# Performance work log

Hardware: AMD Instinct MI355X
Metric: run time of the kernel (lower is better)

The kernel has to match this reference:

```python
import jax, jax.numpy as jnp
import numpy as np

B, S, D = 1, 4096, 512
INNER = 512
K, PAD = 3, 1
MAX_OUT = 4 * S  # static padded output length (torch uses data-dependent max)
EPS = 1e-5
TINY_SLOWDOWN = 0.5


def _conv1d(x, w, b):
    # x: [B, C_in, S], w: [C_out, C_in, K] -> [B, C_out, S]
    y = jax.lax.conv_general_dilated(x, w, window_strides=(1,), padding=[(PAD, PAD)],
                                     dimension_numbers=('NCH', 'OIH', 'NCH'))
    return y + b[None, :, None]


def _layernorm(x, g, b):
    m = jnp.mean(x, axis=-1, keepdims=True)
    v = jnp.var(x, axis=-1, keepdims=True)
    return (x - m) * jax.lax.rsqrt(v + EPS) * g + b


def _duration_predictor(enc, c1w, c1b, g1, b1, c2w, c2b, g2, b2, lw, lb):
    # enc: [B, S, D]; dropout is identity (eval mode)
    x = _conv1d(enc.transpose(0, 2, 1), c1w, c1b).transpose(0, 2, 1)   # [B,S,INNER]
    x = jax.nn.relu(_layernorm(x, g1, b1))
    x = _conv1d(x.transpose(0, 2, 1), c2w, c2b).transpose(0, 2, 1)     # [B,S,INNER]
    x = jax.nn.relu(_layernorm(x, g2, b2))
    out = jax.nn.relu(jnp.einsum('bsd,od->bso', x, lw) + lb)           # [B,S,1]
    return out[..., 0]                                                  # [B,S] (B==1 => matches squeeze/unsqueeze(0))


def setup_inputs() -> dict:
    key = jax.random.key(0)
    ks = jax.random.split(key, 4)
    return {
        'enc_output': jax.random.normal(ks[0], (B, S, D), dtype=jnp.float32),
        'conv1_w': jax.random.normal(ks[1], (INNER, D, K), dtype=jnp.float32) * 0.02,
        'conv1_b': jnp.zeros((INNER,), jnp.float32),
        'ln1_g': jnp.ones((INNER,), jnp.float32),
        'ln1_b': jnp.zeros((INNER,), jnp.float32),
        'conv2_w': jax.random.normal(ks[2], (INNER, INNER, K), dtype=jnp.float32) * 0.02,
        'conv2_b': jnp.zeros((INNER,), jnp.float32),
        'ln2_g': jnp.ones((INNER,), jnp.float32),
        'ln2_b': jnp.zeros((INNER,), jnp.float32),
        'lin_w': jax.random.normal(ks[3], (1, INNER), jnp.float32) * 0.1,
        'lin_b': jnp.zeros((1,), jnp.float32),
    }


def reference(enc_output, conv1_w, conv1_b, ln1_g, ln1_b, conv2_w, conv2_b,
              ln2_g, ln2_b, lin_w, lin_b):
    pred = _duration_predictor(enc_output, conv1_w, conv1_b, ln1_g, ln1_b,
                               conv2_w, conv2_b, ln2_g, ln2_b, lin_w, lin_b)
    dur = jnp.floor(pred + TINY_SLOWDOWN).astype(jnp.int32)            # [B,S], nonneg so floor == int()
    cum = jnp.cumsum(dur, axis=-1)                                     # [B,S]
    t = jnp.arange(MAX_OUT, dtype=jnp.int32)                           # [T]
    # frame t belongs to phoneme i where cum[i-1] <= t < cum[i]
    idx = jax.vmap(lambda c: jnp.searchsorted(c, t, side='right'))(cum)  # [B,T]
    valid = t[None, :] < cum[:, -1:]                                   # [B,T]
    idx = jnp.clip(idx, 0, S - 1)
    gathered = jnp.take_along_axis(enc_output, idx[:, :, None], axis=1)  # [B,T,D]
    mod_enc_output = jnp.where(valid[:, :, None], gathered, jnp.zeros((), enc_output.dtype))
    output_pos = jnp.arange(1, MAX_OUT + 1, dtype=jnp.int64 if jax.config.jax_enable_x64 else jnp.int32)[None, :]
    return mod_enc_output, output_pos
```

## Files before the change

kernel.cpp:

```cpp
#include <hip/hip_runtime.h>

#define S      4096
#define D      512
#define KWIN   3
#define SP     (S + 2)
#define MAXOUT 16384
#define EPSLN  1e-5f
#define NIT    16
#define NKT    48
#define KSPLIT 2
#define KHALF  (NKT / KSPLIT)

typedef __attribute__((ext_vector_type(8)))  short short8;
typedef __attribute__((ext_vector_type(16))) float floatx16;

__device__ inline ushort f2bf(float x) {
  union { float f; unsigned u; } v; v.f = x;
  unsigned r = v.u + 0x7fffu + ((v.u >> 16) & 1u);
  return (ushort)(r >> 16);
}
__device__ inline float bf2f(ushort h) {
  union { float f; unsigned u; } v; v.u = ((unsigned)h) << 16;
  return v.f;
}

#define NB0 1025
#define NB1 384
#define NB3 4

__device__ inline void wpack8(const float* __restrict__ w, ushort* __restrict__ bh,
                              ushort* __restrict__ bl, int q) {
  const int kk0 = (q & 3) * 8;
  const int o   = (q >> 2) & 511;
  const int it  = (q >> 11) & 15;
  const int k   = q >> 15;
  short8 h8, l8;
#pragma unroll
  for (int j = 0; j < 8; ++j) {
    const float v = w[o * (D * KWIN) + (it * 32 + kk0 + j) * KWIN + k];
    const ushort hi = f2bf(v);
    h8[j] = (short)hi;
    l8[j] = (short)f2bf(v - bf2f(hi));
  }
  *(short8*)(bh + (size_t)q * 8) = h8;
  *(short8*)(bl + (size_t)q * 8) = l8;
}

__global__ __launch_bounds__(256) void pack_all_kernel(
    const float* __restrict__ x, const float* __restrict__ w1,
    const float* __restrict__ w2, ushort* __restrict__ Xph,
    ushort* __restrict__ Xpl, ushort* __restrict__ B1h, ushort* __restrict__ B1l,
    ushort* __restrict__ B2h, ushort* __restrict__ B2l,
    ushort* __restrict__ T1h, ushort* __restrict__ T1l) {
  const int b = blockIdx.x;
  if (b < NB0) {
    const int t = b * 256 + threadIdx.x;
    if (t >= SP * 64) return;
    const int g  = t >> 6;
    const int i0 = (t & 63) * 8;
    float vv[8] = {};
    if (g > 0 && g < SP - 1) {
      const float4 v0 = *(const float4*)(x + (size_t)(g - 1) * D + i0);
      const float4 v1 = *(const float4*)(x + (size_t)(g - 1) * D + i0 + 4);
      vv[0] = v0.x; vv[1] = v0.y; vv[2] = v0.z; vv[3] = v0.w;
      vv[4] = v1.x; vv[5] = v1.y; vv[6] = v1.z; vv[7] = v1.w;
    }
    short8 h8, l8;
#pragma unroll
    for (int j = 0; j < 8; ++j) {
      const ushort hi = f2bf(vv[j]);
      h8[j] = (short)hi;
      l8[j] = (short)f2bf(vv[j] - bf2f(hi));
    }
    const size_t dst = ((size_t)(i0 >> 5) * SP + g) * 32 + (i0 & 31);
    *(short8*)(Xph + dst) = h8;
    *(short8*)(Xpl + dst) = l8;
  } else if (b < NB0 + NB1) {
    wpack8(w1, B1h, B1l, (b - NB0) * 256 + threadIdx.x);
  } else if (b < NB0 + 2 * NB1) {
    wpack8(w2, B2h, B2l, (b - NB0 - NB1) * 256 + threadIdx.x);
  } else {
    const int idx = (b - NB0 - 2 * NB1) * 256 + threadIdx.x;
    const int c   = idx >> 6;
    const int rr  = (idx >> 5) & 1;
    const int col = idx & 31;
    const size_t off = ((size_t)c * SP + (rr ? (SP - 1) : 0)) * 32 + col;
    T1h[off] = 0;
    T1l[off] = 0;
  }
}

__device__ inline void gload16(const void* g, void* l) {
  __builtin_amdgcn_global_load_lds((const __attribute__((address_space(1))) void*)g,
                                   (__attribute__((address_space(3))) void*)l,
                                   16, 0, 0);
}

__global__ __launch_bounds__(256) void gemm_mfma_kernel(
    const ushort* __restrict__ Ah, const ushort* __restrict__ Al,
    const ushort* __restrict__ Bh, const ushort* __restrict__ Bl,
    float* __restrict__ C0, float* __restrict__ C1) {
  __shared__ __align__(16) ushort smem[2][4][128 * 32];

  const int tid  = threadIdx.x;
  const int wave = tid >> 6;
  const int lane = tid & 63;
  const int row0 = blockIdx.x * 128;
  const int col0 = blockIdx.y * 128;
  const int ktb  = blockIdx.z * KHALF;
  const int wm0  = (wave >> 1) * 64;
  const int wn0  = (wave & 1) * 64;
  const int ln31 = lane & 31;
  const int half = lane >> 5;

  floatx16 acc[2][2] = {};

  auto stage = [&](int stg, int db) {
    const int kt    = ktb + stg;
    const int tap   = kt >> 4;
    const int itile = kt & 15;
    const ushort* gb;
    if (wave == 0)      gb = Ah + ((size_t)itile * SP + row0 + tap) * 32;
    else if (wave == 1) gb = Al + ((size_t)itile * SP + row0 + tap) * 32;
    else if (wave == 2) gb = Bh + ((size_t)kt * D + col0) * 32;
    else                gb = Bl + ((size_t)kt * D + col0) * 32;
    ushort* lb = &smem[db][wave][0];
#pragma unroll
    for (int seg = 0; seg < 8; ++seg) {
      const int r = seg * 16 + (lane >> 2);
      const int c = (lane & 3) ^ (r & 3);
      gload16(gb + (size_t)r * 32 + c * 8, lb + seg * 512);
    }
  };

  stage(0, 0);

  for (int p = 0; p < KHALF; ++p) {
    const int db = p & 1;
    __syncthreads();
    if (p + 1 < KHALF) stage(p + 1, db ^ 1);

#pragma unroll
    for (int sub = 0; sub < 2; ++sub) {
      const int cchunk = sub * 2 + half;
      short8 ah[2], al2[2], bh[2], bl2[2];
#pragma unroll
      for (int mf = 0; mf < 2; ++mf) {
        const int r  = wm0 + mf * 32 + ln31;
        const int cs = cchunk ^ (r & 3);
        const int off = r * 32 + cs * 8;
        ah[mf]  = *(const short8*)&smem[db][0][off];
        al2[mf] = *(const short8*)&smem[db][1][off];
      }
#pragma unroll
      for (int nf = 0; nf < 2; ++nf) {
        const int r  = wn0 + nf * 32 + ln31;
        const int cs = cchunk ^ (r & 3);
        const int off = r * 32 + cs * 8;
        bh[nf]  = *(const short8*)&smem[db][2][off];
        bl2[nf] = *(const short8*)&smem[db][3][off];
      }
#pragma unroll
      for (int mf = 0; mf < 2; ++mf)
#pragma unroll
        for (int nf = 0; nf < 2; ++nf) {
          acc[mf][nf] = __builtin_amdgcn_mfma_f32_32x32x16_bf16(ah[mf],  bh[nf],  acc[mf][nf], 0, 0, 0);
          acc[mf][nf] = __builtin_amdgcn_mfma_f32_32x32x16_bf16(ah[mf],  bl2[nf], acc[mf][nf], 0, 0, 0);
          acc[mf][nf] = __builtin_amdgcn_mfma_f32_32x32x16_bf16(al2[mf], bh[nf],  acc[mf][nf], 0, 0, 0);
        }
    }
  }

  float* C = (blockIdx.z == 0) ? C0 : C1;
#pragma unroll
  for (int mf = 0; mf < 2; ++mf)
#pragma unroll
    for (int nf = 0; nf < 2; ++nf) {
      const int col = col0 + wn0 + nf * 32 + ln31;
#pragma unroll
      for (int reg = 0; reg < 16; ++reg) {
        const int row = row0 + wm0 + mf * 32 + (reg & 3) + 8 * (reg >> 2) + 4 * half;
        C[(size_t)row * D + col] = acc[mf][nf][reg];
      }
    }
}

__global__ __launch_bounds__(256) void ln_relu_pack_kernel(
    const float* __restrict__ X0, const float* __restrict__ X1,
    const float* __restrict__ cb, const float* __restrict__ gam,
    const float* __restrict__ bet, ushort* __restrict__ th,
    ushort* __restrict__ tl) {
  const int wave = threadIdx.x >> 6;
  const int lane = threadIdx.x & 63;
  const int s = blockIdx.x * 4 + wave;
  const float4* x0p = (const float4*)(X0 + (size_t)s * D);
  const float4* x1p = (const float4*)(X1 + (size_t)s * D);
  const float4 a0 = x0p[2 * lane],     b0 = x0p[2 * lane + 1];
  const float4 a1 = x1p[2 * lane],     b1 = x1p[2 * lane + 1];
  const float4 ca  = ((const float4*)cb)[2 * lane];
  const float4 cb2 = ((const float4*)cb)[2 * lane + 1];
  float v[8] = {(a0.x + a1.x) + ca.x,  (a0.y + a1.y) + ca.y,
                (a0.z + a1.z) + ca.z,  (a0.w + a1.w) + ca.w,
                (b0.x + b1.x) + cb2.x, (b0.y + b1.y) + cb2.y,
                (b0.z + b1.z) + cb2.z, (b0.w + b1.w) + cb2.w};
  float sum = 0.f;
#pragma unroll
  for (int i = 0; i < 8; ++i) sum += v[i];
#pragma unroll
  for (int off = 32; off > 0; off >>= 1) sum += __shfl_xor(sum, off);
  const float m = sum * (1.0f / D);
  float sq = 0.f;
#pragma unroll
  for (int i = 0; i < 8; ++i) { v[i] -= m; sq += v[i] * v[i]; }
#pragma unroll
  for (int off = 32; off > 0; off >>= 1) sq += __shfl_xor(sq, off);
  const float rs = rsqrtf(sq * (1.0f / D) + EPSLN);
  const float4 ga = ((const float4*)gam)[2 * lane];
  const float4 gb = ((const float4*)gam)[2 * lane + 1];
  const float4 ba = ((const float4*)bet)[2 * lane];
  const float4 bb = ((const float4*)bet)[2 * lane + 1];
  const float gg[8] = {ga.x, ga.y, ga.z, ga.w, gb.x, gb.y, gb.z, gb.w};
  const float bt[8] = {ba.x, ba.y, ba.z, ba.w, bb.x, bb.y, bb.z, bb.w};
  short8 h8, l8;
#pragma unroll
  for (int i = 0; i < 8; ++i) {
    const float y = fmaxf(v[i] * rs * gg[i] + bt[i], 0.0f);
    const ushort hi = f2bf(y);
    h8[i] = (short)hi;
    l8[i] = (short)f2bf(y - bf2f(hi));
  }
  const size_t base = ((size_t)(lane >> 2) * SP + (s + 1)) * 32 + (size_t)(lane & 3) * 8;
  *(short8*)(th + base) = h8;
  *(short8*)(tl + base) = l8;
}

__global__ __launch_bounds__(256) void ln2_pred_kernel(
    const float* __restrict__ X0, const float* __restrict__ X1,
    const float* __restrict__ cb, const float* __restrict__ gam,
    const float* __restrict__ bet, const float* __restrict__ lw,
    const float* __restrict__ lb, int* __restrict__ dur) {
  const int wave = threadIdx.x >> 6;
  const int lane = threadIdx.x & 63;
  const int s = blockIdx.x * 4 + wave;
  const float4* x0p = (const float4*)(X0 + (size_t)s * D);
  const float4* x1p = (const float4*)(X1 + (size_t)s * D);
  const float4 a0 = x0p[2 * lane],     b0 = x0p[2 * lane + 1];
  const float4 a1 = x1p[2 * lane],     b1 = x1p[2 * lane + 1];
  const float4 ca  = ((const float4*)cb)[2 * lane];
  const float4 cb2 = ((const float4*)cb)[2 * lane + 1];
  float v[8] = {(a0.x + a1.x) + ca.x,  (a0.y + a1.y) + ca.y,
                (a0.z + a1.z) + ca.z,  (a0.w + a1.w) + ca.w,
                (b0.x + b1.x) + cb2.x, (b0.y + b1.y) + cb2.y,
                (b0.z + b1.z) + cb2.z, (b0.w + b1.w) + cb2.w};
  float sum = 0.f;
#pragma unroll
  for (int i = 0; i < 8; ++i) sum += v[i];
#pragma unroll
  for (int off = 32; off > 0; off >>= 1) sum += __shfl_xor(sum, off);
  const float m = sum * (1.0f / D);
  float sq = 0.f;
#pragma unroll
  for (int i = 0; i < 8; ++i) { v[i] -= m; sq += v[i] * v[i]; }
#pragma unroll
  for (int off = 32; off > 0; off >>= 1) sq += __shfl_xor(sq, off);
  const float rs = rsqrtf(sq * (1.0f / D) + EPSLN);
  const float4 ga = ((const float4*)gam)[2 * lane];
  const float4 gb = ((const float4*)gam)[2 * lane + 1];
  const float4 ba = ((const float4*)bet)[2 * lane];
  const float4 bb = ((const float4*)bet)[2 * lane + 1];
  const float gg[8] = {ga.x, ga.y, ga.z, ga.w, gb.x, gb.y, gb.z, gb.w};
  const float bt[8] = {ba.x, ba.y, ba.z, ba.w, bb.x, bb.y, bb.z, bb.w};
  const float4 w0 = ((const float4*)lw)[2 * lane];
  const float4 w1 = ((const float4*)lw)[2 * lane + 1];
  const float ww[8] = {w0.x, w0.y, w0.z, w0.w, w1.x, w1.y, w1.z, w1.w};
  float d = 0.f;
#pragma unroll
  for (int i = 0; i < 8; ++i) {
    const float y = fmaxf(v[i] * rs * gg[i] + bt[i], 0.0f);
    d += y * ww[i];
  }
#pragma unroll
  for (int off = 32; off > 0; off >>= 1) d += __shfl_xor(d, off);
  if (lane == 0) {
    const float p = fmaxf(d + lb[0], 0.0f);
    dur[s] = (int)floorf(p + 0.5f);
  }
}

__global__ __launch_bounds__(64) void scan_kernel(const int* __restrict__ dur,
                                                  int* __restrict__ cum) {
  const int lane = threadIdx.x;
  const int4* src = (const int4*)dur + (size_t)lane * 16;
  int4 v[16];
  int run = 0;
#pragma unroll
  for (int i = 0; i < 16; ++i) {
    int4 d = src[i];
    d.x += run; d.y += d.x; d.z += d.y; d.w += d.z;
    run = d.w;
    v[i] = d;
  }
  int sc = run;
#pragma unroll
  for (int off = 1; off < 64; off <<= 1) {
    const int n = __shfl_up(sc, off);
    if (lane >= off) sc += n;
  }
  const int base = sc - run;
  int4* dst = (int4*)cum + (size_t)lane * 16;
#pragma unroll
  for (int i = 0; i < 16; ++i) {
    int4 d = v[i];
    d.x += base; d.y += base; d.z += base; d.w += base;
    dst[i] = d;
  }
}

__global__ __launch_bounds__(256) void gather_kernel(
    const float* __restrict__ enc, const int* __restrict__ cum,
    float* __restrict__ out0, float* __restrict__ out1) {
  const int half = threadIdx.x >> 7;
  const int d4   = (threadIdx.x & 127) << 2;
  const int t    = blockIdx.x * 2 + half;
  const int total = cum[S - 1];

  int lo = 0, hi = S;
  while (lo < hi) {
    const int mid = (lo + hi) >> 1;
    if (cum[mid] <= t) lo = mid + 1; else hi = mid;
  }
  const int idx = (lo < S) ? lo : (S - 1);

  float4 v = make_float4(0.f, 0.f, 0.f, 0.f);
  if (t < total) v = *(const float4*)(enc + (size_t)idx * D + d4);
  *(float4*)(out0 + (size_t)t * D + d4) = v;

  if ((threadIdx.x & 127) == 0) out1[t] = (float)(t + 1);
}

extern "C" void kernel_launch(void* const* d_in, const int* in_sizes, int n_in,
                              void* d_out, int out_size, void* d_ws, size_t ws_size,
                              hipStream_t stream) {
  const float* enc = (const float*)d_in[0];
  const float* w1  = (const float*)d_in[1];
  const float* cb1 = (const float*)d_in[2];
  const float* g1  = (const float*)d_in[3];
  const float* be1 = (const float*)d_in[4];
  const float* w2  = (const float*)d_in[5];
  const float* cb2 = (const float*)d_in[6];
  const float* g2  = (const float*)d_in[7];
  const float* be2 = (const float*)d_in[8];
  const float* lw  = (const float*)d_in[9];
  const float* lb  = (const float*)d_in[10];

  float* out0 = (float*)d_out;
  float* out1 = out0 + (size_t)MAXOUT * D;

  const size_t NP = (size_t)NIT * SP * 32;
  const size_t NB = (size_t)NKT * D * 32;
  ushort* Xph = (ushort*)d_ws;
  ushort* Xpl = Xph + NP;
  ushort* T1h = Xpl + NP;
  ushort* T1l = T1h + NP;
  ushort* B1h = T1l + NP;
  ushort* B1l = B1h + NB;
  ushort* B2h = B1l + NB;
  ushort* B2l = B2h + NB;
  float*  t0a = (float*)(B2l + NB);
  float*  t0b = t0a + (size_t)S * D;
  int*   dur  = (int*)(t0b + (size_t)S * D);
  int*   cum  = dur + S;

  pack_all_kernel<<<NB0 + 2 * NB1 + NB3, 256, 0, stream>>>(
      enc, w1, w2, Xph, Xpl, B1h, B1l, B2h, B2l, T1h, T1l);
  gemm_mfma_kernel<<<dim3(S / 128, D / 128, KSPLIT), 256, 0, stream>>>(
      Xph, Xpl, B1h, B1l, t0a, t0b);
  ln_relu_pack_kernel<<<S / 4, 256, 0, stream>>>(t0a, t0b, cb1, g1, be1, T1h, T1l);
  gemm_mfma_kernel<<<dim3(S / 128, D / 128, KSPLIT), 256, 0, stream>>>(
      T1h, T1l, B2h, B2l, t0a, t0b);
  ln2_pred_kernel<<<S / 4, 256, 0, stream>>>(t0a, t0b, cb2, g2, be2, lw, lb, dur);
  scan_kernel<<<1, 64, 0, stream>>>(dur, cum);
  gather_kernel<<<MAXOUT / 2, 256, 0, stream>>>(enc, cum, out0, out1);
}
```

Measured before the change: 170.6 us.

## Split GEMM K dimension four ways and switch LDS tile to column-chunk layout

Raises the split-K factor from 2 to 4, so each GEMM launches 512 blocks instead of 256 and can fill more compute units. The LN kernels now sum four partial outputs. The LDS staging layout changes from a per-row XOR-swizzled layout to a chunk-major layout, so each lane reads 16 contiguous bytes per row. The cost is twice as much fp32 partial-result traffic to and from global memory, plus a different LDS bank-access pattern.

```diff
diff --git a/kernel.cpp b/kernel.cpp
--- a/kernel.cpp
+++ b/kernel.cpp
@@ -8,8 +8,8 @@
 #define EPSLN  1e-5f
 #define NIT    16
 #define NKT    48
-#define KSPLIT 2
-#define KHALF  (NKT / KSPLIT)
+#define KSPLIT 4
+#define KQ     (NKT / KSPLIT)
 
 typedef __attribute__((ext_vector_type(8)))  short short8;
 typedef __attribute__((ext_vector_type(16))) float floatx16;
@@ -99,15 +99,15 @@
 __global__ __launch_bounds__(256) void gemm_mfma_kernel(
     const ushort* __restrict__ Ah, const ushort* __restrict__ Al,
     const ushort* __restrict__ Bh, const ushort* __restrict__ Bl,
-    float* __restrict__ C0, float* __restrict__ C1) {
-  __shared__ __align__(16) ushort smem[2][4][128 * 32];
+    float* __restrict__ Cpart) {
+  __shared__ __align__(16) ushort smem[2][4][4096];
 
   const int tid  = threadIdx.x;
   const int wave = tid >> 6;
   const int lane = tid & 63;
   const int row0 = blockIdx.x * 128;
   const int col0 = blockIdx.y * 128;
-  const int ktb  = blockIdx.z * KHALF;
+  const int ktb  = blockIdx.z * KQ;
   const int wm0  = (wave >> 1) * 64;
   const int wn0  = (wave & 1) * 64;
   const int ln31 = lane & 31;
@@ -127,38 +127,38 @@
     ushort* lb = &smem[db][wave][0];
 #pragma unroll
     for (int seg = 0; seg < 8; ++seg) {
-      const int r = seg * 16 + (lane >> 2);
-      const int c = (lane & 3) ^ (r & 3);
+      const int r = (seg & 1) * 64 + lane;
+      const int c = seg >> 1;
       gload16(gb + (size_t)r * 32 + c * 8, lb + seg * 512);
     }
   };
 
   stage(0, 0);
 
-  for (int p = 0; p < KHALF; ++p) {
+  for (int p = 0; p < KQ; ++p) {
     const int db = p & 1;
     __syncthreads();
-    if (p + 1 < KHALF) stage(p + 1, db ^ 1);
-
+    if (p + 1 < KQ) stage(p + 1, db ^ 1);
+
+    const ushort* Ahs = &smem[db][0][0];
+    const ushort* Als = &smem[db][1][0];
+    const ushort* Bhs = &smem[db][2][0];
+    const ushort* Bls = &smem[db][3][0];
 #pragma unroll
     for (int sub = 0; sub < 2; ++sub) {
-      const int cchunk = sub * 2 + half;
+      const int cc = sub * 2 + half;
       short8 ah[2], al2[2], bh[2], bl2[2];
 #pragma unroll
       for (int mf = 0; mf < 2; ++mf) {
-        const int r  = wm0 + mf * 32 + ln31;
-        const int cs = cchunk ^ (r & 3);
-        const int off = r * 32 + cs * 8;
-        ah[mf]  = *(const short8*)&smem[db][0][off];
-        al2[mf] = *(const short8*)&smem[db][1][off];
+        const int off = (cc * 128 + wm0 + mf * 32 + ln31) * 8;
+        ah[mf]  = *(const short8*)&Ahs[off];
+        al2[mf] = *(const short8*)&Als[off];
       }
 #pragma unroll
       for (int nf = 0; nf < 2; ++nf) {
-        const int r  = wn0 + nf * 32 + ln31;
-        const int cs = cchunk ^ (r & 3);
-        const int off = r * 32 + cs * 8;
-        bh[nf]  = *(const short8*)&smem[db][2][off];
-        bl2[nf] = *(const short8*)&smem[db][3][off];
+        const int off = (cc * 128 + wn0 + nf * 32 + ln31) * 8;
+        bh[nf]  = *(const short8*)&Bhs[off];
+        bl2[nf] = *(const short8*)&Bls[off];
       }
 #pragma unroll
       for (int mf = 0; mf < 2; ++mf)
@@ -171,7 +171,7 @@
     }
   }
 
-  float* C = (blockIdx.z == 0) ? C0 : C1;
+  float* C = Cpart + (size_t)blockIdx.z * S * D;
 #pragma unroll
   for (int mf = 0; mf < 2; ++mf)
 #pragma unroll
@@ -185,24 +185,28 @@
     }
 }
 
+__device__ inline void load8(const float* p, int lane, float o[8]) {
+  const float4 a = ((const float4*)p)[2 * lane];
+  const float4 b = ((const float4*)p)[2 * lane + 1];
+  o[0] = a.x; o[1] = a.y; o[2] = a.z; o[3] = a.w;
+  o[4] = b.x; o[5] = b.y; o[6] = b.z; o[7] = b.w;
+}
+
 __global__ __launch_bounds__(256) void ln_relu_pack_kernel(
-    const float* __restrict__ X0, const float* __restrict__ X1,
-    const float* __restrict__ cb, const float* __restrict__ gam,
-    const float* __restrict__ bet, ushort* __restrict__ th,
-    ushort* __restrict__ tl) {
+    const float* __restrict__ Xp, const float* __restrict__ cb,
+    const float* __restrict__ gam, const float* __restrict__ bet,
+    ushort* __restrict__ th, ushort* __restrict__ tl) {
   const int wave = threadIdx.x >> 6;
   const int lane = threadIdx.x & 63;
   const int s = blockIdx.x * 4 + wave;
-  const float4* x0p = (const float4*)(X0 + (size_t)s * D);
-  const float4* x1p = (const float4*)(X1 + (size_t)s * D);
-  const float4 a0 = x0p[2 * lane],     b0 = x0p[2 * lane + 1];
-  const float4 a1 = x1p[2 * lane],     b1 = x1p[2 * lane + 1];
-  const float4 ca  = ((const float4*)cb)[2 * lane];
-  const float4 cb2 = ((const float4*)cb)[2 * lane + 1];
-  float v[8] = {(a0.x + a1.x) + ca.x,  (a0.y + a1.y) + ca.y,
-                (a0.z + a1.z) + ca.z,  (a0.w + a1.w) + ca.w,
-                (b0.x + b1.x) + cb2.x, (b0.y + b1.y) + cb2.y,
-                (b0.z + b1.z) + cb2.z, (b0.w + b1.w) + cb2.w};
+  float v[8], x1[8], x2[8], x3[8], bi[8];
+  load8(Xp + (size_t)s * D, lane, v);
+  load8(Xp + (size_t)S * D + (size_t)s * D, lane, x1);
+  load8(Xp + 2 * (size_t)S * D + (size_t)s * D, lane, x2);
+  load8(Xp + 3 * (size_t)S * D + (size_t)s * D, lane, x3);
+  load8(cb, lane, bi);
+#pragma unroll
+  for (int i = 0; i < 8; ++i) v[i] = ((v[i] + x1[i]) + (x2[i] + x3[i])) + bi[i];
   float sum = 0.f;
 #pragma unroll
   for (int i = 0; i < 8; ++i) sum += v[i];
@@ -215,12 +219,9 @@
 #pragma unroll
   for (int off = 32; off > 0; off >>= 1) sq += __shfl_xor(sq, off);
   const float rs = rsqrtf(sq * (1.0f / D) + EPSLN);
-  const float4 ga = ((const float4*)gam)[2 * lane];
-  const float4 gb = ((const float4*)gam)[2 * lane + 1];
-  const float4 ba = ((const float4*)bet)[2 * lane];
-  const float4 bb = ((const float4*)bet)[2 * lane + 1];
-  const float gg[8] = {ga.x, ga.y, ga.z, ga.w, gb.x, gb.y, gb.z, gb.w};
-  const float bt[8] = {ba.x, ba.y, ba.z, ba.w, bb.x, bb.y, bb.z, bb.w};
+  float gg[8], bt[8];
+  load8(gam, lane, gg);
+  load8(bet, lane, bt);
   short8 h8, l8;
 #pragma unroll
   for (int i = 0; i < 8; ++i) {
@@ -235,23 +236,21 @@
 }
 
 __global__ __launch_bounds__(256) void ln2_pred_kernel(
-    const float* __restrict__ X0, const float* __restrict__ X1,
-    const float* __restrict__ cb, const float* __restrict__ gam,
-    const float* __restrict__ bet, const float* __restrict__ lw,
-    const float* __restrict__ lb, int* __restrict__ dur) {
+    const float* __restrict__ Xp, const float* __restrict__ cb,
+    const float* __restrict__ gam, const float* __restrict__ bet,
+    const float* __restrict__ lw, const float* __restrict__ lb,
+    int* __restrict__ dur) {
   const int wave = threadIdx.x >> 6;
   const int lane = threadIdx.x & 63;
   const int s = blockIdx.x * 4 + wave;
-  const float4* x0p = (const float4*)(X0 + (size_t)s * D);
-  const float4* x1p = (const float4*)(X1 + (size_t)s * D);
-  const float4 a0 = x0p[2 * lane],     b0 = x0p[2 * lane + 1];
-  const float4 a1 = x1p[2 * lane],     b1 = x1p[2 * lane + 1];
-  const float4 ca  = ((const float4*)cb)[2 * lane];
-  const float4 cb2 = ((const float4*)cb)[2 * lane + 1];
-  float v[8] = {(a0.x + a1.x) + ca.x,  (a0.y + a1.y) + ca.y,
-                (a0.z + a1.z) + ca.z,  (a0.w + a1.w) + ca.w,
-                (b0.x + b1.x) + cb2.x, (b0.y + b1.y) + cb2.y,
-                (b0.z + b1.z) + cb2.z, (b0.w + b1.w) + cb2.w};
+  float v[8], x1[8], x2[8], x3[8], bi[8];
+  load8(Xp + (size_t)s * D, lane, v);
+  load8(Xp + (size_t)S * D + (size_t)s * D, lane, x1);
+  load8(Xp + 2 * (size_t)S * D + (size_t)s * D, lane, x2);
+  load8(Xp + 3 * (size_t)S * D + (size_t)s * D, lane, x3);
+  load8(cb, lane, bi);
+#pragma unroll
+  for (int i = 0; i < 8; ++i) v[i] = ((v[i] + x1[i]) + (x2[i] + x3[i])) + bi[i];
   float sum = 0.f;
 #pragma unroll
   for (int i = 0; i < 8; ++i) sum += v[i];
@@ -264,15 +263,10 @@
 #pragma unroll
   for (int off = 32; off > 0; off >>= 1) sq += __shfl_xor(sq, off);
   const float rs = rsqrtf(sq * (1.0f / D) + EPSLN);
-  const float4 ga = ((const float4*)gam)[2 * lane];
-  const float4 gb = ((const float4*)gam)[2 * lane + 1];
-  const float4 ba = ((const float4*)bet)[2 * lane];
-  const float4 bb = ((const float4*)bet)[2 * lane + 1];
-  const float gg[8] = {ga.x, ga.y, ga.z, ga.w, gb.x, gb.y, gb.z, gb.w};
-  const float bt[8] = {ba.x, ba.y, ba.z, ba.w, bb.x, bb.y, bb.z, bb.w};
-  const float4 w0 = ((const float4*)lw)[2 * lane];
-  const float4 w1 = ((const float4*)lw)[2 * lane + 1];
-  const float ww[8] = {w0.x, w0.y, w0.z, w0.w, w1.x, w1.y, w1.z, w1.w};
+  float gg[8], bt[8], ww[8];
+  load8(gam, lane, gg);
+  load8(bet, lane, bt);
+  load8(lw, lane, ww);
   float d = 0.f;
 #pragma unroll
   for (int i = 0; i < 8; ++i) {
@@ -366,19 +360,18 @@
   ushort* B1l = B1h + NB;
   ushort* B2h = B1l + NB;
   ushort* B2l = B2h + NB;
-  float*  t0a = (float*)(B2l + NB);
-  float*  t0b = t0a + (size_t)S * D;
-  int*   dur  = (int*)(t0b + (size_t)S * D);
+  float*  t0  = (float*)(B2l + NB);
+  int*   dur  = (int*)(t0 + (size_t)KSPLIT * S * D);
   int*   cum  = dur + S;
 
   pack_all_kernel<<<NB0 + 2 * NB1 + NB3, 256, 0, stream>>>(
       enc, w1, w2, Xph, Xpl, B1h, B1l, B2h, B2l, T1h, T1l);
   gemm_mfma_kernel<<<dim3(S / 128, D / 128, KSPLIT), 256, 0, stream>>>(
-      Xph, Xpl, B1h, B1l, t0a, t0b);
-  ln_relu_pack_kernel<<<S / 4, 256, 0, stream>>>(t0a, t0b, cb1, g1, be1, T1h, T1l);
+      Xph, Xpl, B1h, B1l, t0);
+  ln_relu_pack_kernel<<<S / 4, 256, 0, stream>>>(t0, cb1, g1, be1, T1h, T1l);
   gemm_mfma_kernel<<<dim3(S / 128, D / 128, KSPLIT), 256, 0, stream>>>(
-      T1h, T1l, B2h, B2l, t0a, t0b);
-  ln2_pred_kernel<<<S / 4, 256, 0, stream>>>(t0a, t0b, cb2, g2, be2, lw, lb, dur);
+      T1h, T1l, B2h, B2l, t0);
+  ln2_pred_kernel<<<S / 4, 256, 0, stream>>>(t0, cb2, g2, be2, lw, lb, dur);
   scan_kernel<<<1, 64, 0, stream>>>(dur, cum);
   gather_kernel<<<MAXOUT / 2, 256, 0, stream>>>(enc, cum, out0, out1);
 }
```

Result: slower. 178.9 us (+4.9%).
